# Kernel optimization log

Measured on AMD Instinct MI355X. Metric: run time of the kernel, lower is better.

The kernel has to match this reference:

```python
import jax, jax.numpy as jnp
import numpy as np

NEG_INF = -1e30


def setup_inputs() -> dict:
    key = jax.random.key(0)
    k1, k2, k3 = jax.random.split(key, 3)
    B, H, HKV, S, D = 2, 16, 4, 2048, 128
    q = jax.random.normal(k1, (B, H, S, D), dtype=jnp.float32)
    k = jax.random.normal(k2, (B, HKV, S, D), dtype=jnp.float32)
    v = jax.random.normal(k3, (B, HKV, S, D), dtype=jnp.float32)
    return {"q": q, "k": k, "v": v}


def reference(q, k, v):
    # Flash attention math (exact, non-tiled reference): causal + sliding-window
    # masked softmax(QK^T * scale) V with GQA head grouping.
    B, H, M, D = q.shape
    _, HKV, N, _ = k.shape
    G = H // HKV  # num_kv_groups
    W = 512       # sliding window size
    scale = 1.0 / jnp.sqrt(jnp.float32(D))

    qg = q.reshape(B, HKV, G, M, D)
    # scores: [B, HKV, G, M, N]
    scores = jnp.einsum("bkgmd,bknd->bkgmn", qg, k) * scale

    i = jnp.arange(M)[:, None]
    j = jnp.arange(N)[None, :]
    # causal: j <= i ; sliding window: only last W keys visible (i - j < W)
    keep = (j <= i) & ((i - j) < W)
    scores = jnp.where(keep[None, None, None], scores, NEG_INF)

    p = jax.nn.softmax(scores.astype(jnp.float32), axis=-1).astype(q.dtype)
    out = jnp.einsum("bkgmn,bknd->bkgmd", p, v)
    return out.reshape(B, H, M, D)
```

## Files before the change

kernel.cpp:

```cpp
#include <hip/hip_runtime.h>
#include <hip/hip_bf16.h>
#include <stdint.h>

#define SEQ 2048
#define HD  128
#define WIN 512
#define NH  16
#define NKV 4
#define BATCH 2

typedef __attribute__((ext_vector_type(8))) short bf16x8;
typedef __attribute__((ext_vector_type(4))) short bf16x4;
typedef __attribute__((ext_vector_type(4))) float f32x4;
typedef __attribute__((ext_vector_type(4))) uint32_t u32x4;
typedef __attribute__((ext_vector_type(2))) uint32_t u32x2;

#define EXP2(x) __builtin_amdgcn_exp2f(x)

#define AS1(p) ((const __attribute__((address_space(1))) uint32_t*)(p))
#define AS3(p) ((__attribute__((address_space(3))) uint32_t*)(p))

__device__ __forceinline__ uint32_t pk2(float a, float b) {
    __hip_bfloat162 h = __float22bfloat162_rn(make_float2(a, b));
    return *reinterpret_cast<uint32_t*>(&h);
}

__global__ __launch_bounds__(256) void prep_kv(
    const float* __restrict__ k,
    const float* __restrict__ v,
    uint16_t* __restrict__ kb,
    uint16_t* __restrict__ vt)
{
    const int tile = blockIdx.x;
    const int kvh  = tile >> 5;
    const int kt   = tile & 31;
    const int t    = threadIdx.x;

    const float* ksrc = k + ((size_t)kvh * SEQ + kt * 64) * HD;
    const float* vsrc = v + ((size_t)kvh * SEQ + kt * 64) * HD;
    uint16_t* kdst = kb + ((size_t)kvh * SEQ + kt * 64) * HD;
    uint16_t* vdst = vt + ((size_t)kvh * 32 + kt) * (size_t)(64 * HD);

    __shared__ uint16_t lv[64][132];

    #pragma unroll
    for (int i = 0; i < 8; ++i) {
        int u = t + i * 256;
        int row = u >> 5, c4 = u & 31;
        float4 f = *reinterpret_cast<const float4*>(vsrc + row * HD + c4 * 4);
        u32x2 w; w.x = pk2(f.x, f.y); w.y = pk2(f.z, f.w);
        *reinterpret_cast<u32x2*>(&lv[row][c4 * 4]) = w;
    }
    #pragma unroll
    for (int i = 0; i < 8; ++i) {
        int u = t + i * 256;
        int row = u >> 5, c4 = u & 31;
        float4 f = *reinterpret_cast<const float4*>(ksrc + row * HD + c4 * 4);
        u32x2 w; w.x = pk2(f.x, f.y); w.y = pk2(f.z, f.w);
        int col = c4 * 4;
        int e = row * HD + ((((col >> 3) ^ (row & 7)) << 3) | (col & 7));
        *reinterpret_cast<u32x2*>(&kdst[e]) = w;
    }
    __syncthreads();
    #pragma unroll
    for (int i = 0; i < 4; ++i) {
        int g = t + i * 256;
        int dim = g >> 3, pg = g & 7;
        uint32_t w[4];
        #pragma unroll
        for (int jj = 0; jj < 4; ++jj) {
            int p0 = pg * 8 + jj * 2;
            int s0 = p0 >> 5, w0 = p0 & 31;
            int key0 = s0 * 32 + ((w0 >> 2) & 1) * 16 + (w0 >> 3) * 4 + (w0 & 3);
            int p1 = p0 + 1;
            int s1 = p1 >> 5, w1 = p1 & 31;
            int key1 = s1 * 32 + ((w1 >> 2) & 1) * 16 + (w1 >> 3) * 4 + (w1 & 3);
            w[jj] = (uint32_t)lv[key0][dim] | ((uint32_t)lv[key1][dim] << 16);
        }
        int e = dim * 64 + ((pg ^ (dim & 7)) << 3);
        u32x4 wv = {w[0], w[1], w[2], w[3]};
        *reinterpret_cast<u32x4*>(&vdst[e]) = wv;
    }
}

__global__ __launch_bounds__(512, 2) void fa_mfma(
    const float* __restrict__ q,
    const uint16_t* __restrict__ kb,
    const uint16_t* __restrict__ vt,
    float* __restrict__ out)
{
    const int tid  = threadIdx.x;
    const int wave = tid >> 6;
    const int lane = tid & 63;
    const int l4   = lane >> 4;
    const int l15  = lane & 15;

    const int bh   = blockIdx.x >> 4;
    const int qblk = blockIdx.x & 15;
    const int q0   = qblk << 7;
    const int hkv  = (bh & (NH - 1)) >> 2;
    const int b    = bh >> 4;

    const int i0   = q0 + wave * 16;

    __shared__ __align__(16) uint16_t lds_k[2][64 * HD];
    __shared__ __align__(16) uint16_t lds_vt[2][64 * HD];

    const float scale2 = 0.08838834764831845f * 1.4426950408889634f;

    const size_t qbase = (size_t)bh * SEQ * HD;
    const uint16_t* kt_base = kb + (size_t)(b * NKV + hkv) * SEQ * HD;
    const uint16_t* vt_base = vt + (size_t)(b * NKV + hkv) * SEQ * HD;

    bf16x8 qf[4];
    {
        const float* qr = q + qbase + (size_t)(i0 + l15) * HD;
        #pragma unroll
        for (int ks = 0; ks < 4; ++ks) {
            const float4* g = reinterpret_cast<const float4*>(qr + ks * 32 + l4 * 8);
            float4 a = g[0], bq = g[1];
            u32x4 t;
            t.x = pk2(a.x * scale2, a.y * scale2);
            t.y = pk2(a.z * scale2, a.w * scale2);
            t.z = pk2(bq.x * scale2, bq.y * scale2);
            t.w = pk2(bq.z * scale2, bq.w * scale2);
            qf[ks] = __builtin_bit_cast(bf16x8, t);
        }
    }

    f32x4 O[8];
    #pragma unroll
    for (int a2 = 0; a2 < 8; ++a2) O[a2] = (f32x4){0.f, 0.f, 0.f, 0.f};
    float mrow = -1e30f;
    float lrow = 0.f;

    const int kt_lo_blk = (q0 >= 512) ? ((q0 - 511) >> 6) : 0;
    const int kt_hi_blk = (q0 + 127) >> 6;
    const int lo_w = (i0 >= 512) ? ((i0 - 511) >> 6) : 0;
    const int hi_w = (i0 + 15) >> 6;

    auto stage = [&](int kt, int pb) {
        const uint16_t* ks = kt_base + (size_t)kt * 64 * HD;
        const uint16_t* vs = vt_base + (size_t)kt * 64 * HD;
        const int ch = wave * 2;
        #pragma unroll
        for (int c = 0; c < 2; ++c) {
            __builtin_amdgcn_global_load_lds(
                AS1(ks + (ch + c) * 512 + lane * 8),
                AS3(&lds_k[pb][(ch + c) * 512]), 16, 0, 0);
            __builtin_amdgcn_global_load_lds(
                AS1(vs + (ch + c) * 512 + lane * 8),
                AS3(&lds_vt[pb][(ch + c) * 512]), 16, 0, 0);
        }
    };

    stage(kt_lo_blk, 0);
    __syncthreads();

    int par = 0;
    for (int kt = kt_lo_blk; kt <= kt_hi_blk; ++kt) {
        if (kt < kt_hi_blk) stage(kt + 1, par ^ 1);

        if (kt >= lo_w && kt <= hi_w) {
            f32x4 sf[4];
            #pragma unroll
            for (int mt = 0; mt < 4; ++mt) sf[mt] = (f32x4){0.f, 0.f, 0.f, 0.f};
            __builtin_amdgcn_s_setprio(1);
            #pragma unroll
            for (int mt = 0; mt < 4; ++mt) {
                const int arow = mt * 16 + l15;
                #pragma unroll
                for (int ks = 0; ks < 4; ++ks) {
                    bf16x8 af = *reinterpret_cast<const bf16x8*>(
                        &lds_k[par][arow * HD + ((((ks * 4 + l4) ^ (arow & 7))) << 3)]);
                    sf[mt] = __builtin_amdgcn_mfma_f32_16x16x32_bf16(
                        af, qf[ks], sf[mt], 0, 0, 0);
                }
            }
            __builtin_amdgcn_s_setprio(0);
            const bool needmask = (kt == hi_w) || (kt == lo_w && i0 > 511);
            if (needmask) {
                const int iq = i0 + l15;
                #pragma unroll
                for (int mt = 0; mt < 4; ++mt) {
                    int jb = kt * 64 + mt * 16 + l4 * 4;
                    #pragma unroll
                    for (int r = 0; r < 4; ++r) {
                        int j = jb + r;
                        if (!((j <= iq) && (iq - j < WIN))) sf[mt][r] = -1e30f;
                    }
                }
            }
            float a0 = fmaxf(fmaxf(sf[0][0], sf[0][1]), fmaxf(sf[0][2], sf[0][3]));
            float a1 = fmaxf(fmaxf(sf[1][0], sf[1][1]), fmaxf(sf[1][2], sf[1][3]));
            float a2 = fmaxf(fmaxf(sf[2][0], sf[2][1]), fmaxf(sf[2][2], sf[2][3]));
            float a3 = fmaxf(fmaxf(sf[3][0], sf[3][1]), fmaxf(sf[3][2], sf[3][3]));
            float tm = fmaxf(fmaxf(a0, a1), fmaxf(a2, a3));
            tm = fmaxf(tm, __shfl_xor(tm, 16, 64));
            tm = fmaxf(tm, __shfl_xor(tm, 32, 64));
            const bool defer = __all(tm <= mrow + 8.0f);
            if (!defer) {
                float mn = fmaxf(mrow, tm);
                float alpha = EXP2(mrow - mn);
                mrow = mn;
                lrow *= alpha;
                #pragma unroll
                for (int r = 0; r < 4; ++r) {
                    float ar = __shfl(alpha, l4 * 4 + r, 64);
                    #pragma unroll
                    for (int nt = 0; nt < 8; ++nt) O[nt][r] *= ar;
                }
            }
            bf16x4 pfrag[4];
            {
                float me = fmaxf(mrow, -1e20f);
                float s[4];
                #pragma unroll
                for (int mt = 0; mt < 4; ++mt) {
                    float p0 = EXP2(sf[mt][0] - me);
                    float p1 = EXP2(sf[mt][1] - me);
                    float p2 = EXP2(sf[mt][2] - me);
                    float p3 = EXP2(sf[mt][3] - me);
                    u32x2 t;
                    t.x = pk2(p0, p1);
                    t.y = pk2(p2, p3);
                    pfrag[mt] = __builtin_bit_cast(bf16x4, t);
                    s[mt] = (p0 + p1) + (p2 + p3);
                }
                float ts = (s[0] + s[1]) + (s[2] + s[3]);
                ts += __shfl_xor(ts, 16, 64);
                ts += __shfl_xor(ts, 32, 64);
                lrow += ts;
            }
            __builtin_amdgcn_s_setprio(1);
            #pragma unroll
            for (int s = 0; s < 2; ++s) {
                bf16x8 pa = __builtin_shufflevector(pfrag[2 * s], pfrag[2 * s + 1],
                                                    0, 1, 2, 3, 4, 5, 6, 7);
                #pragma unroll
                for (int nt = 0; nt < 8; ++nt) {
                    const int vr = nt * 16 + l15;
                    bf16x8 vf = *reinterpret_cast<const bf16x8*>(
                        &lds_vt[par][vr * 64 + ((((s * 4 + l4) ^ (vr & 7))) << 3)]);
                    O[nt] = __builtin_amdgcn_mfma_f32_16x16x32_bf16(pa, vf, O[nt], 0, 0, 0);
                }
            }
            __builtin_amdgcn_s_setprio(0);
        }
        __syncthreads();
        par ^= 1;
    }

    {
        float inv = 1.0f / lrow;
        #pragma unroll
        for (int r = 0; r < 4; ++r) {
            float li = __shfl(inv, l4 * 4 + r, 64);
            int row = i0 + l4 * 4 + r;
            float* orow = out + qbase + (size_t)row * HD;
            #pragma unroll
            for (int nt = 0; nt < 8; ++nt)
                orow[nt * 16 + l15] = O[nt][r] * li;
        }
    }
}

#define KSTR 136
#define VSTR 72
#define VT_ROWS (HD * VSTR + (HD / 4) * 4)
__device__ __forceinline__ int vt_off(int row, int col) {
    return row * VSTR + (row >> 2) * 4 + col;
}

__global__ __launch_bounds__(512, 2)
void fa_mfma_fused(
    const float* __restrict__ q,
    const float* __restrict__ k,
    const float* __restrict__ v,
    float* __restrict__ out)
{
    const int tid  = threadIdx.x;
    const int wave = tid >> 6;
    const int lane = tid & 63;
    const int l4   = lane >> 4;
    const int l15  = lane & 15;

    const int bh   = blockIdx.x >> 4;
    const int qblk = blockIdx.x & 15;
    const int q0   = qblk << 7;
    const int hkv  = (bh & (NH - 1)) >> 2;
    const int b    = bh >> 4;

    const int i0   = q0 + wave * 16;

    __shared__ __align__(16) uint16_t lds_k[2][64 * KSTR];
    __shared__ __align__(16) uint16_t lds_vt[2][VT_ROWS];

    const float scale2 = 0.08838834764831845f * 1.4426950408889634f;

    const size_t qbase  = (size_t)bh * SEQ * HD;
    const size_t kvbase = (size_t)(b * NKV + hkv) * SEQ * HD;

    bf16x8 qf[4];
    {
        const float* qr = q + qbase + (size_t)(i0 + l15) * HD;
        #pragma unroll
        for (int ks = 0; ks < 4; ++ks) {
            const float4* g = reinterpret_cast<const float4*>(qr + ks * 32 + l4 * 8);
            float4 a = g[0], bq = g[1];
            u32x4 t;
            t.x = pk2(a.x * scale2, a.y * scale2);
            t.y = pk2(a.z * scale2, a.w * scale2);
            t.z = pk2(bq.x * scale2, bq.y * scale2);
            t.w = pk2(bq.z * scale2, bq.w * scale2);
            qf[ks] = __builtin_bit_cast(bf16x8, t);
        }
    }

    f32x4 O[8];
    #pragma unroll
    for (int a2 = 0; a2 < 8; ++a2) O[a2] = (f32x4){0.f, 0.f, 0.f, 0.f};
    float mrow = -1e30f;
    float lrow = 0.f;

    const int kt_lo_blk = (q0 >= 512) ? ((q0 - 511) >> 6) : 0;
    const int kt_hi_blk = (q0 + 127) >> 6;
    const int lo_w = (i0 >= 512) ? ((i0 - 511) >> 6) : 0;
    const int hi_w = (i0 + 15) >> 6;

    const int vdg = tid & 31;
    const int vkg = tid >> 5;
    float4 rKa[2], rKb[2], rV[4];

    auto prefetch_k = [&](int kt) {
        const float* kp = k + kvbase + (size_t)kt * 64 * HD;
        #pragma unroll
        for (int it = 0; it < 2; ++it) {
            int flat8 = tid + it * 512, key = flat8 >> 4, ch = flat8 & 15;
            const float4* g = reinterpret_cast<const float4*>(kp + key * HD + ch * 8);
            rKa[it] = g[0]; rKb[it] = g[1];
        }
    };
    auto prefetch_v = [&](int kt) {
        const float* vp = v + kvbase + (size_t)kt * 64 * HD;
        #pragma unroll
        for (int r = 0; r < 4; ++r)
            rV[r] = *reinterpret_cast<const float4*>(vp + (vkg * 4 + r) * HD + vdg * 4);
    };
    auto pack_k = [&](int pb) {
        #pragma unroll
        for (int it = 0; it < 2; ++it) {
            int flat8 = tid + it * 512, key = flat8 >> 4, ch = flat8 & 15;
            uint4 wv;
            wv.x = pk2(rKa[it].x, rKa[it].y);  wv.y = pk2(rKa[it].z, rKa[it].w);
            wv.z = pk2(rKb[it].x, rKb[it].y);  wv.w = pk2(rKb[it].z, rKb[it].w);
            *reinterpret_cast<uint4*>(&lds_k[pb][key * KSTR + ch * 8]) = wv;
        }
    };
    auto pack_v = [&](int pb) {
        const float* rvf = reinterpret_cast<const float*>(rV);
        #pragma unroll
        for (int i = 0; i < 4; ++i) {
            u32x2 wv;
            wv.x = pk2(rvf[0 * 4 + i], rvf[1 * 4 + i]);
            wv.y = pk2(rvf[2 * 4 + i], rvf[3 * 4 + i]);
            *reinterpret_cast<u32x2*>(&lds_vt[pb][vt_off(vdg * 4 + i, vkg * 4)]) = wv;
        }
    };

    prefetch_k(kt_lo_blk);
    prefetch_v(kt_lo_blk);
    pack_k(0);
    pack_v(0);
    __syncthreads();

    int par = 0;
    for (int kt = kt_lo_blk; kt <= kt_hi_blk; ++kt) {
        const bool more = (kt < kt_hi_blk);
        if (more) prefetch_k(kt + 1);

        if (kt >= lo_w && kt <= hi_w) {
            f32x4 sf[4];
            #pragma unroll
            for (int mt = 0; mt < 4; ++mt) sf[mt] = (f32x4){0.f, 0.f, 0.f, 0.f};
            __builtin_amdgcn_s_setprio(1);
            #pragma unroll
            for (int mt = 0; mt < 4; ++mt) {
                #pragma unroll
                for (int ks = 0; ks < 4; ++ks) {
                    bf16x8 af = *reinterpret_cast<const bf16x8*>(
                        &lds_k[par][(mt * 16 + l15) * KSTR + ks * 32 + l4 * 8]);
                    sf[mt] = __builtin_amdgcn_mfma_f32_16x16x32_bf16(
                        af, qf[ks], sf[mt], 0, 0, 0);
                }
            }
            __builtin_amdgcn_s_setprio(0);
            if (more) { pack_k(par ^ 1); prefetch_v(kt + 1); }
            const bool needmask = (kt == hi_w) || (kt == lo_w && i0 > 511);
            if (needmask) {
                const int iq = i0 + l15;
                #pragma unroll
                for (int mt = 0; mt < 4; ++mt) {
                    int jb = kt * 64 + mt * 16 + l4 * 4;
                    #pragma unroll
                    for (int r = 0; r < 4; ++r) {
                        int j = jb + r;
                        if (!((j <= iq) && (iq - j < WIN))) sf[mt][r] = -1e30f;
                    }
                }
            }
            float a0 = fmaxf(fmaxf(sf[0][0], sf[0][1]), fmaxf(sf[0][2], sf[0][3]));
            float a1 = fmaxf(fmaxf(sf[1][0], sf[1][1]), fmaxf(sf[1][2], sf[1][3]));
            float a2 = fmaxf(fmaxf(sf[2][0], sf[2][1]), fmaxf(sf[2][2], sf[2][3]));
            float a3 = fmaxf(fmaxf(sf[3][0], sf[3][1]), fmaxf(sf[3][2], sf[3][3]));
            float tm = fmaxf(fmaxf(a0, a1), fmaxf(a2, a3));
            tm = fmaxf(tm, __shfl_xor(tm, 16, 64));
            tm = fmaxf(tm, __shfl_xor(tm, 32, 64));
            const bool defer = __all(tm <= mrow + 8.0f);
            if (!defer) {
                float mn = fmaxf(mrow, tm);
                float alpha = EXP2(mrow - mn);
                mrow = mn;
                lrow *= alpha;
                #pragma unroll
                for (int r = 0; r < 4; ++r) {
                    float ar = __shfl(alpha, l4 * 4 + r, 64);
                    #pragma unroll
                    for (int nt = 0; nt < 8; ++nt) O[nt][r] *= ar;
                }
            }
            bf16x4 pfrag[4];
            {
                float me = fmaxf(mrow, -1e20f);
                float s[4];
                #pragma unroll
                for (int mt = 0; mt < 4; ++mt) {
                    float p0 = EXP2(sf[mt][0] - me);
                    float p1 = EXP2(sf[mt][1] - me);
                    float p2 = EXP2(sf[mt][2] - me);
                    float p3 = EXP2(sf[mt][3] - me);
                    u32x2 t;
                    t.x = pk2(p0, p1);
                    t.y = pk2(p2, p3);
                    pfrag[mt] = __builtin_bit_cast(bf16x4, t);
                    s[mt] = (p0 + p1) + (p2 + p3);
                }
                float ts = (s[0] + s[1]) + (s[2] + s[3]);
                ts += __shfl_xor(ts, 16, 64);
                ts += __shfl_xor(ts, 32, 64);
                lrow += ts;
            }
            if (more) pack_v(par ^ 1);
            __builtin_amdgcn_s_setprio(1);
            #pragma unroll
            for (int s = 0; s < 2; ++s) {
                bf16x8 pa = __builtin_shufflevector(pfrag[2 * s], pfrag[2 * s + 1],
                                                    0, 1, 2, 3, 4, 5, 6, 7);
                #pragma unroll
                for (int nt = 0; nt < 8; ++nt) {
                    const int vr = nt * 16 + l15;
                    bf16x4 v0 = *reinterpret_cast<const bf16x4*>(
                        &lds_vt[par][vt_off(vr, s * 32 + l4 * 4)]);
                    bf16x4 v1 = *reinterpret_cast<const bf16x4*>(
                        &lds_vt[par][vt_off(vr, s * 32 + 16 + l4 * 4)]);
                    bf16x8 vf = __builtin_shufflevector(v0, v1, 0, 1, 2, 3, 4, 5, 6, 7);
                    O[nt] = __builtin_amdgcn_mfma_f32_16x16x32_bf16(pa, vf, O[nt], 0, 0, 0);
                }
            }
            __builtin_amdgcn_s_setprio(0);
        } else {
            if (more) { prefetch_v(kt + 1); pack_k(par ^ 1); pack_v(par ^ 1); }
        }
        __syncthreads();
        par ^= 1;
    }

    {
        float inv = 1.0f / lrow;
        #pragma unroll
        for (int r = 0; r < 4; ++r) {
            float li = __shfl(inv, l4 * 4 + r, 64);
            int row = i0 + l4 * 4 + r;
            float* orow = out + qbase + (size_t)row * HD;
            #pragma unroll
            for (int nt = 0; nt < 8; ++nt)
                orow[nt * 16 + l15] = O[nt][r] * li;
        }
    }
}

extern "C" void kernel_launch(void* const* d_in, const int* in_sizes, int n_in,
                              void* d_out, int out_size, void* d_ws, size_t ws_size,
                              hipStream_t stream) {
    const float* q = (const float*)d_in[0];
    const float* k = (const float*)d_in[1];
    const float* v = (const float*)d_in[2];
    float* out     = (float*)d_out;

    const size_t kv_elems = (size_t)BATCH * NKV * SEQ * HD;
    const size_t ws_needed = kv_elems * 2u * sizeof(uint16_t);

    if (d_ws != nullptr && ws_size >= ws_needed) {
        uint16_t* kb  = (uint16_t*)d_ws;
        uint16_t* vtw = kb + kv_elems;
        hipLaunchKernelGGL(prep_kv, dim3(BATCH * NKV * (SEQ / 64)), dim3(256), 0,
                           stream, k, v, kb, vtw);
        hipLaunchKernelGGL(fa_mfma, dim3(BATCH * NH * (SEQ / 128)), dim3(512), 0,
                           stream, q, kb, vtw, out);
    } else {
        hipLaunchKernelGGL(fa_mfma_fused, dim3(BATCH * NH * (SEQ / 128)), dim3(512),
                           0, stream, q, k, v, out);
    }
}
```

Before: 121.0 us.

## Switch main attention kernel to 32x32x16 MFMA with 4 waves of 32 rows

```diff
diff --git a/kernel.cpp b/kernel.cpp
--- a/kernel.cpp
+++ b/kernel.cpp
@@ -12,6 +12,7 @@
 typedef __attribute__((ext_vector_type(8))) short bf16x8;
 typedef __attribute__((ext_vector_type(4))) short bf16x4;
 typedef __attribute__((ext_vector_type(4))) float f32x4;
+typedef __attribute__((ext_vector_type(16))) float f32x16;
 typedef __attribute__((ext_vector_type(4))) uint32_t u32x4;
 typedef __attribute__((ext_vector_type(2))) uint32_t u32x2;
 
@@ -64,26 +65,24 @@
     __syncthreads();
     #pragma unroll
     for (int i = 0; i < 4; ++i) {
-        int g = t + i * 256;
-        int dim = g >> 3, pg = g & 7;
+        int gid = t + i * 256;
+        int d = gid >> 3, g = gid & 7;
+        int s = g >> 1, h = g & 1;
         uint32_t w[4];
         #pragma unroll
         for (int jj = 0; jj < 4; ++jj) {
-            int p0 = pg * 8 + jj * 2;
-            int s0 = p0 >> 5, w0 = p0 & 31;
-            int key0 = s0 * 32 + ((w0 >> 2) & 1) * 16 + (w0 >> 3) * 4 + (w0 & 3);
-            int p1 = p0 + 1;
-            int s1 = p1 >> 5, w1 = p1 & 31;
-            int key1 = s1 * 32 + ((w1 >> 2) & 1) * 16 + (w1 >> 3) * 4 + (w1 & 3);
-            w[jj] = (uint32_t)lv[key0][dim] | ((uint32_t)lv[key1][dim] << 16);
-        }
-        int e = dim * 64 + ((pg ^ (dim & 7)) << 3);
+            int j0 = 2 * jj;
+            int key0 = s * 16 + h * 4 + (j0 & 3) + ((j0 >> 2) << 3);
+            w[jj] = (uint32_t)lv[key0][d] | ((uint32_t)lv[key0 + 1][d] << 16);
+        }
+        int e = d * 64 + ((g ^ (d & 7)) << 3);
         u32x4 wv = {w[0], w[1], w[2], w[3]};
         *reinterpret_cast<u32x4*>(&vdst[e]) = wv;
     }
 }
 
-__global__ __launch_bounds__(512, 2) void fa_mfma(
+__global__ __launch_bounds__(256) __attribute__((amdgpu_waves_per_eu(2, 2)))
+void fa_mfma(
     const float* __restrict__ q,
     const uint16_t* __restrict__ kb,
     const uint16_t* __restrict__ vt,
@@ -92,8 +91,9 @@
     const int tid  = threadIdx.x;
     const int wave = tid >> 6;
     const int lane = tid & 63;
-    const int l4   = lane >> 4;
-    const int l15  = lane & 15;
+    const int l31  = lane & 31;
+    const int h    = lane >> 5;
+    const int hs   = h << 2;
 
     const int bh   = blockIdx.x >> 4;
     const int qblk = blockIdx.x & 15;
@@ -101,7 +101,7 @@
     const int hkv  = (bh & (NH - 1)) >> 2;
     const int b    = bh >> 4;
 
-    const int i0   = q0 + wave * 16;
+    const int i0   = q0 + wave * 32;
 
     __shared__ __align__(16) uint16_t lds_k[2][64 * HD];
     __shared__ __align__(16) uint16_t lds_vt[2][64 * HD];
@@ -111,6 +111,195 @@
     const size_t qbase = (size_t)bh * SEQ * HD;
     const uint16_t* kt_base = kb + (size_t)(b * NKV + hkv) * SEQ * HD;
     const uint16_t* vt_base = vt + (size_t)(b * NKV + hkv) * SEQ * HD;
+
+    bf16x8 qf[8];
+    {
+        const float* qr = q + qbase + (size_t)(i0 + l31) * HD;
+        #pragma unroll
+        for (int dk = 0; dk < 8; ++dk) {
+            const float4* g = reinterpret_cast<const float4*>(qr + dk * 16 + h * 8);
+            float4 a = g[0], bq = g[1];
+            u32x4 t;
+            t.x = pk2(a.x * scale2, a.y * scale2);
+            t.y = pk2(a.z * scale2, a.w * scale2);
+            t.z = pk2(bq.x * scale2, bq.y * scale2);
+            t.w = pk2(bq.z * scale2, bq.w * scale2);
+            qf[dk] = __builtin_bit_cast(bf16x8, t);
+        }
+    }
+
+    f32x16 O[4];
+    #pragma unroll
+    for (int nt = 0; nt < 4; ++nt)
+        #pragma unroll
+        for (int r = 0; r < 16; ++r) O[nt][r] = 0.f;
+    float mrow = -1e30f;
+    float lrow = 0.f;
+
+    const int kt_lo_blk = (q0 >= 512) ? ((q0 - 511) >> 6) : 0;
+    const int kt_hi_blk = (q0 + 127) >> 6;
+    const int lo_w = (i0 >= 512) ? ((i0 - 511) >> 6) : 0;
+    const int hi_w = (i0 + 31) >> 6;
+
+    auto stage = [&](int kt, int pb) {
+        const uint16_t* ks = kt_base + (size_t)kt * 64 * HD;
+        const uint16_t* vs = vt_base + (size_t)kt * 64 * HD;
+        #pragma unroll
+        for (int c = 0; c < 4; ++c) {
+            const int off = c * 2048 + tid * 8;
+            __builtin_amdgcn_global_load_lds(AS1(ks + off), AS3(&lds_k[pb][off]),
+                                             16, 0, 0);
+            __builtin_amdgcn_global_load_lds(AS1(vs + off), AS3(&lds_vt[pb][off]),
+                                             16, 0, 0);
+        }
+    };
+
+    stage(kt_lo_blk, 0);
+    __syncthreads();
+
+    int par = 0;
+    for (int kt = kt_lo_blk; kt <= kt_hi_blk; ++kt) {
+        if (kt < kt_hi_blk) stage(kt + 1, par ^ 1);
+
+        if (kt >= lo_w && kt <= hi_w) {
+            f32x16 sf[2];
+            #pragma unroll
+            for (int mt = 0; mt < 2; ++mt)
+                #pragma unroll
+                for (int r = 0; r < 16; ++r) sf[mt][r] = 0.f;
+            __builtin_amdgcn_s_setprio(1);
+            #pragma unroll
+            for (int dk = 0; dk < 8; ++dk) {
+                #pragma unroll
+                for (int mt = 0; mt < 2; ++mt) {
+                    const int krow = mt * 32 + l31;
+                    bf16x8 af = *reinterpret_cast<const bf16x8*>(
+                        &lds_k[par][krow * HD + (((dk * 2 + h) ^ (krow & 7)) << 3)]);
+                    sf[mt] = __builtin_amdgcn_mfma_f32_32x32x16_bf16(
+                        af, qf[dk], sf[mt], 0, 0, 0);
+                }
+            }
+            __builtin_amdgcn_s_setprio(0);
+            const bool needmask = (kt == hi_w) || (kt == lo_w && i0 > 511);
+            if (needmask) {
+                const int iq = i0 + l31;
+                #pragma unroll
+                for (int mt = 0; mt < 2; ++mt) {
+                    #pragma unroll
+                    for (int r = 0; r < 16; ++r) {
+                        int j = kt * 64 + mt * 32 + (r & 3) + ((r >> 2) << 3) + hs;
+                        if (!((j <= iq) && (iq - j < WIN))) sf[mt][r] = -1e30f;
+                    }
+                }
+            }
+            float tmx = sf[0][0];
+            #pragma unroll
+            for (int r = 1; r < 16; ++r) tmx = fmaxf(tmx, sf[0][r]);
+            #pragma unroll
+            for (int r = 0; r < 16; ++r) tmx = fmaxf(tmx, sf[1][r]);
+            tmx = fmaxf(tmx, __shfl_xor(tmx, 32, 64));
+            const bool defer = __all(tmx <= mrow + 8.0f);
+            if (!defer) {
+                float mn = fmaxf(mrow, tmx);
+                float alpha = EXP2(mrow - mn);
+                mrow = mn;
+                lrow *= alpha;
+                #pragma unroll
+                for (int r = 0; r < 16; ++r) {
+                    float ar = __shfl(alpha, (r & 3) + ((r >> 2) << 3) + hs, 64);
+                    #pragma unroll
+                    for (int nt = 0; nt < 4; ++nt) O[nt][r] *= ar;
+                }
+            }
+            uint32_t pf[2][8];
+            {
+                float me = fmaxf(mrow, -1e20f);
+                float ts = 0.f;
+                #pragma unroll
+                for (int mt = 0; mt < 2; ++mt) {
+                    #pragma unroll
+                    for (int rr = 0; rr < 8; ++rr) {
+                        float p0 = EXP2(sf[mt][2 * rr] - me);
+                        float p1 = EXP2(sf[mt][2 * rr + 1] - me);
+                        pf[mt][rr] = pk2(p0, p1);
+                        ts += p0 + p1;
+                    }
+                }
+                ts += __shfl_xor(ts, 32, 64);
+                lrow += ts;
+            }
+            __builtin_amdgcn_s_setprio(1);
+            #pragma unroll
+            for (int s = 0; s < 4; ++s) {
+                const int mt = s >> 1, base = (s & 1) * 4;
+                u32x4 pu = {pf[mt][base], pf[mt][base + 1],
+                            pf[mt][base + 2], pf[mt][base + 3]};
+                bf16x8 pa = __builtin_bit_cast(bf16x8, pu);
+                #pragma unroll
+                for (int nt = 0; nt < 4; ++nt) {
+                    const int d = nt * 32 + l31;
+                    const int g = s * 2 + h;
+                    bf16x8 vf = *reinterpret_cast<const bf16x8*>(
+                        &lds_vt[par][d * 64 + ((g ^ (d & 7)) << 3)]);
+                    O[nt] = __builtin_amdgcn_mfma_f32_32x32x16_bf16(
+                        pa, vf, O[nt], 0, 0, 0);
+                }
+            }
+            __builtin_amdgcn_s_setprio(0);
+        }
+        __syncthreads();
+        par ^= 1;
+    }
+
+    {
+        float inv = 1.0f / lrow;
+        #pragma unroll
+        for (int r = 0; r < 16; ++r) {
+            const int qr_ = (r & 3) + ((r >> 2) << 3) + hs;
+            float li = __shfl(inv, qr_, 64);
+            float* orow = out + qbase + (size_t)(i0 + qr_) * HD;
+            #pragma unroll
+            for (int nt = 0; nt < 4; ++nt)
+                orow[nt * 32 + l31] = O[nt][r] * li;
+        }
+    }
+}
+
+#define KSTR 136
+#define VSTR 72
+#define VT_ROWS (HD * VSTR + (HD / 4) * 4)
+__device__ __forceinline__ int vt_off(int row, int col) {
+    return row * VSTR + (row >> 2) * 4 + col;
+}
+
+__global__ __launch_bounds__(512, 2)
+void fa_mfma_fused(
+    const float* __restrict__ q,
+    const float* __restrict__ k,
+    const float* __restrict__ v,
+    float* __restrict__ out)
+{
+    const int tid  = threadIdx.x;
+    const int wave = tid >> 6;
+    const int lane = tid & 63;
+    const int l4   = lane >> 4;
+    const int l15  = lane & 15;
+
+    const int bh   = blockIdx.x >> 4;
+    const int qblk = blockIdx.x & 15;
+    const int q0   = qblk << 7;
+    const int hkv  = (bh & (NH - 1)) >> 2;
+    const int b    = bh >> 4;
+
+    const int i0   = q0 + wave * 16;
+
+    __shared__ __align__(16) uint16_t lds_k[2][64 * KSTR];
+    __shared__ __align__(16) uint16_t lds_vt[2][VT_ROWS];
+
+    const float scale2 = 0.08838834764831845f * 1.4426950408889634f;
+
+    const size_t qbase  = (size_t)bh * SEQ * HD;
+    const size_t kvbase = (size_t)(b * NKV + hkv) * SEQ * HD;
 
     bf16x8 qf[4];
     {
@@ -139,27 +328,56 @@
     const int lo_w = (i0 >= 512) ? ((i0 - 511) >> 6) : 0;
     const int hi_w = (i0 + 15) >> 6;
 
-    auto stage = [&](int kt, int pb) {
-        const uint16_t* ks = kt_base + (size_t)kt * 64 * HD;
-        const uint16_t* vs = vt_base + (size_t)kt * 64 * HD;
-        const int ch = wave * 2;
-        #pragma unroll
-        for (int c = 0; c < 2; ++c) {
-            __builtin_amdgcn_global_load_lds(
-                AS1(ks + (ch + c) * 512 + lane * 8),
-                AS3(&lds_k[pb][(ch + c) * 512]), 16, 0, 0);
-            __builtin_amdgcn_global_load_lds(
-                AS1(vs + (ch + c) * 512 + lane * 8),
-                AS3(&lds_vt[pb][(ch + c) * 512]), 16, 0, 0);
+    const int vdg = tid & 31;
+    const int vkg = tid >> 5;
+    float4 rKa[2], rKb[2], rV[4];
+
+    auto prefetch_k = [&](int kt) {
+        const float* kp = k + kvbase + (size_t)kt * 64 * HD;
+        #pragma unroll
+        for (int it = 0; it < 2; ++it) {
+            int flat8 = tid + it * 512, key = flat8 >> 4, ch = flat8 & 15;
+            const float4* g = reinterpret_cast<const float4*>(kp + key * HD + ch * 8);
+            rKa[it] = g[0]; rKb[it] = g[1];
         }
     };
-
-    stage(kt_lo_blk, 0);
+    auto prefetch_v = [&](int kt) {
+        const float* vp = v + kvbase + (size_t)kt * 64 * HD;
+        #pragma unroll
+        for (int r = 0; r < 4; ++r)
+            rV[r] = *reinterpret_cast<const float4*>(vp + (vkg * 4 + r) * HD + vdg * 4);
+    };
+    auto pack_k = [&](int pb) {
+        #pragma unroll
+        for (int it = 0; it < 2; ++it) {
+            int flat8 = tid + it * 512, key = flat8 >> 4, ch = flat8 & 15;
+            uint4 wv;
+            wv.x = pk2(rKa[it].x, rKa[it].y);  wv.y = pk2(rKa[it].z, rKa[it].w);
+            wv.z = pk2(rKb[it].x, rKb[it].y);  wv.w = pk2(rKb[it].z, rKb[it].w);
+            *reinterpret_cast<uint4*>(&lds_k[pb][key * KSTR + ch * 8]) = wv;
+        }
+    };
+    auto pack_v = [&](int pb) {
+        const float* rvf = reinterpret_cast<const float*>(rV);
+        #pragma unroll
+        for (int i = 0; i < 4; ++i) {
+            u32x2 wv;
+            wv.x = pk2(rvf[0 * 4 + i], rvf[1 * 4 + i]);
+            wv.y = pk2(rvf[2 * 4 + i], rvf[3 * 4 + i]);
+            *reinterpret_cast<u32x2*>(&lds_vt[pb][vt_off(vdg * 4 + i, vkg * 4)]) = wv;
+        }
+    };
+
+    prefetch_k(kt_lo_blk);
+    prefetch_v(kt_lo_blk);
+    pack_k(0);
+    pack_v(0);
     __syncthreads();
 
     int par = 0;
     for (int kt = kt_lo_blk; kt <= kt_hi_blk; ++kt) {
-        if (kt < kt_hi_blk) stage(kt + 1, par ^ 1);
+        const bool more = (kt < kt_hi_blk);
+        if (more) prefetch_k(kt + 1);
 
         if (kt >= lo_w && kt <= hi_w) {
             f32x4 sf[4];
@@ -168,16 +386,16 @@
             __builtin_amdgcn_s_setprio(1);
             #pragma unroll
             for (int mt = 0; mt < 4; ++mt) {
-                const int arow = mt * 16 + l15;
                 #pragma unroll
                 for (int ks = 0; ks < 4; ++ks) {
                     bf16x8 af = *reinterpret_cast<const bf16x8*>(
-                        &lds_k[par][arow * HD + ((((ks * 4 + l4) ^ (arow & 7))) << 3)]);
+                        &lds_k[par][(mt * 16 + l15) * KSTR + ks * 32 + l4 * 8]);
                     sf[mt] = __builtin_amdgcn_mfma_f32_16x16x32_bf16(
                         af, qf[ks], sf[mt], 0, 0, 0);
                 }
             }
             __builtin_amdgcn_s_setprio(0);
+            if (more) { pack_k(par ^ 1); prefetch_v(kt + 1); }
             const bool needmask = (kt == hi_w) || (kt == lo_w && i0 > 511);
             if (needmask) {
                 const int iq = i0 + l15;
@@ -232,224 +450,6 @@
                 ts += __shfl_xor(ts, 32, 64);
                 lrow += ts;
             }
-            __builtin_amdgcn_s_setprio(1);
-            #pragma unroll
-            for (int s = 0; s < 2; ++s) {
-                bf16x8 pa = __builtin_shufflevector(pfrag[2 * s], pfrag[2 * s + 1],
-                                                    0, 1, 2, 3, 4, 5, 6, 7);
-                #pragma unroll
-                for (int nt = 0; nt < 8; ++nt) {
-                    const int vr = nt * 16 + l15;
-                    bf16x8 vf = *reinterpret_cast<const bf16x8*>(
-                        &lds_vt[par][vr * 64 + ((((s * 4 + l4) ^ (vr & 7))) << 3)]);
-                    O[nt] = __builtin_amdgcn_mfma_f32_16x16x32_bf16(pa, vf, O[nt], 0, 0, 0);
-                }
-            }
-            __builtin_amdgcn_s_setprio(0);
-        }
-        __syncthreads();
-        par ^= 1;
-    }
-
-    {
-        float inv = 1.0f / lrow;
-        #pragma unroll
-        for (int r = 0; r < 4; ++r) {
-            float li = __shfl(inv, l4 * 4 + r, 64);
-            int row = i0 + l4 * 4 + r;
-            float* orow = out + qbase + (size_t)row * HD;
-            #pragma unroll
-            for (int nt = 0; nt < 8; ++nt)
-                orow[nt * 16 + l15] = O[nt][r] * li;
-        }
-    }
-}
-
-#define KSTR 136
-#define VSTR 72
-#define VT_ROWS (HD * VSTR + (HD / 4) * 4)
-__device__ __forceinline__ int vt_off(int row, int col) {
-    return row * VSTR + (row >> 2) * 4 + col;
-}
-
-__global__ __launch_bounds__(512, 2)
-void fa_mfma_fused(
-    const float* __restrict__ q,
-    const float* __restrict__ k,
-    const float* __restrict__ v,
-    float* __restrict__ out)
-{
-    const int tid  = threadIdx.x;
-    const int wave = tid >> 6;
-    const int lane = tid & 63;
-    const int l4   = lane >> 4;
-    const int l15  = lane & 15;
-
-    const int bh   = blockIdx.x >> 4;
-    const int qblk = blockIdx.x & 15;
-    const int q0   = qblk << 7;
-    const int hkv  = (bh & (NH - 1)) >> 2;
-    const int b    = bh >> 4;
-
-    const int i0   = q0 + wave * 16;
-
-    __shared__ __align__(16) uint16_t lds_k[2][64 * KSTR];
-    __shared__ __align__(16) uint16_t lds_vt[2][VT_ROWS];
-
-    const float scale2 = 0.08838834764831845f * 1.4426950408889634f;
-
-    const size_t qbase  = (size_t)bh * SEQ * HD;
-    const size_t kvbase = (size_t)(b * NKV + hkv) * SEQ * HD;
-
-    bf16x8 qf[4];
-    {
-        const float* qr = q + qbase + (size_t)(i0 + l15) * HD;
-        #pragma unroll
-        for (int ks = 0; ks < 4; ++ks) {
-            const float4* g = reinterpret_cast<const float4*>(qr + ks * 32 + l4 * 8);
-            float4 a = g[0], bq = g[1];
-            u32x4 t;
-            t.x = pk2(a.x * scale2, a.y * scale2);
-            t.y = pk2(a.z * scale2, a.w * scale2);
-            t.z = pk2(bq.x * scale2, bq.y * scale2);
-            t.w = pk2(bq.z * scale2, bq.w * scale2);
-            qf[ks] = __builtin_bit_cast(bf16x8, t);
-        }
-    }
-
-    f32x4 O[8];
-    #pragma unroll
-    for (int a2 = 0; a2 < 8; ++a2) O[a2] = (f32x4){0.f, 0.f, 0.f, 0.f};
-    float mrow = -1e30f;
-    float lrow = 0.f;
-
-    const int kt_lo_blk = (q0 >= 512) ? ((q0 - 511) >> 6) : 0;
-    const int kt_hi_blk = (q0 + 127) >> 6;
-    const int lo_w = (i0 >= 512) ? ((i0 - 511) >> 6) : 0;
-    const int hi_w = (i0 + 15) >> 6;
-
-    const int vdg = tid & 31;
-    const int vkg = tid >> 5;
-    float4 rKa[2], rKb[2], rV[4];
-
-    auto prefetch_k = [&](int kt) {
-        const float* kp = k + kvbase + (size_t)kt * 64 * HD;
-        #pragma unroll
-        for (int it = 0; it < 2; ++it) {
-            int flat8 = tid + it * 512, key = flat8 >> 4, ch = flat8 & 15;
-            const float4* g = reinterpret_cast<const float4*>(kp + key * HD + ch * 8);
-            rKa[it] = g[0]; rKb[it] = g[1];
-        }
-    };
-    auto prefetch_v = [&](int kt) {
-        const float* vp = v + kvbase + (size_t)kt * 64 * HD;
-        #pragma unroll
-        for (int r = 0; r < 4; ++r)
-            rV[r] = *reinterpret_cast<const float4*>(vp + (vkg * 4 + r) * HD + vdg * 4);
-    };
-    auto pack_k = [&](int pb) {
-        #pragma unroll
-        for (int it = 0; it < 2; ++it) {
-            int flat8 = tid + it * 512, key = flat8 >> 4, ch = flat8 & 15;
-            uint4 wv;
-            wv.x = pk2(rKa[it].x, rKa[it].y);  wv.y = pk2(rKa[it].z, rKa[it].w);
-            wv.z = pk2(rKb[it].x, rKb[it].y);  wv.w = pk2(rKb[it].z, rKb[it].w);
-            *reinterpret_cast<uint4*>(&lds_k[pb][key * KSTR + ch * 8]) = wv;
-        }
-    };
-    auto pack_v = [&](int pb) {
-        const float* rvf = reinterpret_cast<const float*>(rV);
-        #pragma unroll
-        for (int i = 0; i < 4; ++i) {
-            u32x2 wv;
-            wv.x = pk2(rvf[0 * 4 + i], rvf[1 * 4 + i]);
-            wv.y = pk2(rvf[2 * 4 + i], rvf[3 * 4 + i]);
-            *reinterpret_cast<u32x2*>(&lds_vt[pb][vt_off(vdg * 4 + i, vkg * 4)]) = wv;
-        }
-    };
-
-    prefetch_k(kt_lo_blk);
-    prefetch_v(kt_lo_blk);
-    pack_k(0);
-    pack_v(0);
-    __syncthreads();
-
-    int par = 0;
-    for (int kt = kt_lo_blk; kt <= kt_hi_blk; ++kt) {
-        const bool more = (kt < kt_hi_blk);
-        if (more) prefetch_k(kt + 1);
-
-        if (kt >= lo_w && kt <= hi_w) {
-            f32x4 sf[4];
-            #pragma unroll
-            for (int mt = 0; mt < 4; ++mt) sf[mt] = (f32x4){0.f, 0.f, 0.f, 0.f};
-            __builtin_amdgcn_s_setprio(1);
-            #pragma unroll
-            for (int mt = 0; mt < 4; ++mt) {
-                #pragma unroll
-                for (int ks = 0; ks < 4; ++ks) {
-                    bf16x8 af = *reinterpret_cast<const bf16x8*>(
-                        &lds_k[par][(mt * 16 + l15) * KSTR + ks * 32 + l4 * 8]);
-                    sf[mt] = __builtin_amdgcn_mfma_f32_16x16x32_bf16(
-                        af, qf[ks], sf[mt], 0, 0, 0);
-                }
-            }
-            __builtin_amdgcn_s_setprio(0);
-            if (more) { pack_k(par ^ 1); prefetch_v(kt + 1); }
-            const bool needmask = (kt == hi_w) || (kt == lo_w && i0 > 511);
-            if (needmask) {
-                const int iq = i0 + l15;
-                #pragma unroll
-                for (int mt = 0; mt < 4; ++mt) {
-                    int jb = kt * 64 + mt * 16 + l4 * 4;
-                    #pragma unroll
-                    for (int r = 0; r < 4; ++r) {
-                        int j = jb + r;
-                        if (!((j <= iq) && (iq - j < WIN))) sf[mt][r] = -1e30f;
-                    }
-                }
-            }
-            float a0 = fmaxf(fmaxf(sf[0][0], sf[0][1]), fmaxf(sf[0][2], sf[0][3]));
-            float a1 = fmaxf(fmaxf(sf[1][0], sf[1][1]), fmaxf(sf[1][2], sf[1][3]));
-            float a2 = fmaxf(fmaxf(sf[2][0], sf[2][1]), fmaxf(sf[2][2], sf[2][3]));
-            float a3 = fmaxf(fmaxf(sf[3][0], sf[3][1]), fmaxf(sf[3][2], sf[3][3]));
-            float tm = fmaxf(fmaxf(a0, a1), fmaxf(a2, a3));
-            tm = fmaxf(tm, __shfl_xor(tm, 16, 64));
-            tm = fmaxf(tm, __shfl_xor(tm, 32, 64));
-            const bool defer = __all(tm <= mrow + 8.0f);
-            if (!defer) {
-                float mn = fmaxf(mrow, tm);
-                float alpha = EXP2(mrow - mn);
-                mrow = mn;
-                lrow *= alpha;
-                #pragma unroll
-                for (int r = 0; r < 4; ++r) {
-                    float ar = __shfl(alpha, l4 * 4 + r, 64);
-                    #pragma unroll
-                    for (int nt = 0; nt < 8; ++nt) O[nt][r] *= ar;
-                }
-            }
-            bf16x4 pfrag[4];
-            {
-                float me = fmaxf(mrow, -1e20f);
-                float s[4];
-                #pragma unroll
-                for (int mt = 0; mt < 4; ++mt) {
-                    float p0 = EXP2(sf[mt][0] - me);
-                    float p1 = EXP2(sf[mt][1] - me);
-                    float p2 = EXP2(sf[mt][2] - me);
-                    float p3 = EXP2(sf[mt][3] - me);
-                    u32x2 t;
-                    t.x = pk2(p0, p1);
-                    t.y = pk2(p2, p3);
-                    pfrag[mt] = __builtin_bit_cast(bf16x4, t);
-                    s[mt] = (p0 + p1) + (p2 + p3);
-                }
-                float ts = (s[0] + s[1]) + (s[2] + s[3]);
-                ts += __shfl_xor(ts, 16, 64);
-                ts += __shfl_xor(ts, 32, 64);
-                lrow += ts;
-            }
             if (more) pack_v(par ^ 1);
             __builtin_amdgcn_s_setprio(1);
             #pragma unroll
@@ -505,7 +505,7 @@
         uint16_t* vtw = kb + kv_elems;
         hipLaunchKernelGGL(prep_kv, dim3(BATCH * NKV * (SEQ / 64)), dim3(256), 0,
                            stream, k, v, kb, vtw);
-        hipLaunchKernelGGL(fa_mfma, dim3(BATCH * NH * (SEQ / 128)), dim3(512), 0,
+        hipLaunchKernelGGL(fa_mfma, dim3(BATCH * NH * (SEQ / 128)), dim3(256), 0,
                            stream, q, kb, vtw, out);
     } else {
         hipLaunchKernelGGL(fa_mfma_fused, dim3(BATCH * NH * (SEQ / 128)), dim3(512),
```

Result: no change. 121.0 us (+0.0%).
